# Kernel tuning notes

Measured on AMD Instinct MI355X. Metric: run time of the kernel, lower is better.

The kernel has to match this reference:

```python
import jax, jax.numpy as jnp
import numpy as np

H = 2880
E = 8
K = 2
FF = 2880
CLIP = 7.0
AUX_COEF = 0.01
INIT_STD = 0.02
B, T = 2, 1024


def setup_inputs() -> dict:
    key = jax.random.key(0)
    ks = jax.random.split(key, 4)
    x = jax.random.normal(ks[0], (B, T, H), dtype=jnp.float32)
    W_in = INIT_STD * jax.random.normal(ks[1], (E, H, 2 * FF), dtype=jnp.float32)
    b_in = jnp.zeros((E, 2 * FF), dtype=jnp.float32)
    W_out = INIT_STD * jax.random.normal(ks[2], (E, FF, H), dtype=jnp.float32)
    b_out = jnp.zeros((E, H), dtype=jnp.float32)
    router_w = INIT_STD * jax.random.normal(ks[3], (E, H), dtype=jnp.float32)
    router_b = jnp.zeros((E,), dtype=jnp.float32)
    return {"x": x, "W_in": W_in, "b_in": b_in, "W_out": W_out,
            "b_out": b_out, "router_w": router_w, "router_b": router_b}


def reference(x, W_in, b_in, W_out, b_out, router_w, router_b):
    Bx, Tx, Hx = x.shape
    x_flat = x.reshape(-1, Hx)                       # [S, H]
    logits = x_flat @ router_w.T + router_b          # [S, E]

    topk_w, topk_idx = jax.lax.top_k(logits, K)      # [S, K]
    topk_w = jax.nn.softmax(topk_w.astype(jnp.float32), axis=-1).astype(x.dtype)
    one_hot = jax.nn.one_hot(topk_idx, E, dtype=x.dtype)        # [S, K, E]
    final_w = (one_hot * topk_w[..., None]).sum(axis=1)          # [S, E]

    probs = jax.nn.softmax(logits.astype(jnp.float32), axis=-1)  # [S, E]
    importance = probs.mean(axis=0)
    load = final_w.astype(jnp.float32).mean(axis=0)
    aux_loss = AUX_COEF * E * (importance * load).sum()

    # Dense over all experts (as in the original module)
    expert_in = jnp.einsum('sh,ehd->sed', x_flat, W_in) + b_in   # [S, E, 2FF]
    up, gate = jnp.split(expert_in, 2, axis=-1)
    up = jnp.clip(up, -CLIP, CLIP)
    gate = jnp.clip(gate, -CLIP, CLIP)
    act = jax.nn.silu(gate) * up                                 # [S, E, FF]
    expert_out = jnp.einsum('sef,efh->seh', act, W_out) + b_out  # [S, E, H]
    out = jnp.einsum('seh,se->sh', expert_out, final_w).reshape(Bx, Tx, Hx)

    expert_utilization = final_w.mean(axis=0)
    router_entropy = -(probs * jnp.log(probs + 1e-10)).sum(axis=-1).mean()
    return out, aux_loss, expert_utilization, router_entropy
```

## Files before the change

kernel.cpp:

```cpp
#include <hip/hip_runtime.h>
#include <hip/hip_bf16.h>
#include <cstdint>
#include <cstddef>

#define H_ 2880
#define E_ 8
#define FF_ 2880
#define TWO_FF 5760
#define S_ 2048
#define NPAD 5120
#define CLIPV 7.0f
#define AUXC 0.01f
#define NKB 45

#define GRIDP  22112
#define GRID1C 5120
#define GRID2  640

typedef __attribute__((ext_vector_type(8))) short bf16x8;
typedef __attribute__((ext_vector_type(4))) float f32x4;

#define WS_COUNTS   0
#define WS_BASEP    64
#define WS_NS       104
#define WS_SCHED_E  128
#define WS_SCHED_C  5248
#define WS_SCHED_R  10368
#define WS_SCH2_E   15488
#define WS_SCH2_C   18048
#define WS_SCH2_R   20608
#define WS_IDX2     23168
#define WS_W2       39552
#define WS_PROBS    55936
#define WS_ENT      121472
#define WS_TOKL     129664
#define WS_ASSW     150144
#define WS_AG       262144
#define WS_TIN      29753344
#define WS_ACT      295174144
#define WS_TOUT     324665344

typedef const __attribute__((address_space(1))) void global_cvoid;
typedef __attribute__((address_space(3))) void lds_void;

__device__ __forceinline__ void gload_lds16(const void* g, void* l) {
  __builtin_amdgcn_global_load_lds((global_cvoid*)g, (lds_void*)l, 16, 0, 0);
}

__device__ __forceinline__ unsigned int pack2bf(float a, float b) {
  __hip_bfloat162 h = __float22bfloat162_rn(make_float2(a, b));
  union { __hip_bfloat162 h; unsigned int u; } c; c.h = h; return c.u;
}

__device__ __forceinline__ unsigned short f2bf1(float f) {
  __hip_bfloat16 h = __float2bfloat16(f);
  union { __hip_bfloat16 h; unsigned short u; } c; c.h = h; return c.u;
}

__device__ __forceinline__ int xcd_lid(int bid, int ns) {
  int q = ns >> 3, r = ns & 7;
  int xcd = bid & 7, i = bid >> 3;
  int cnt = q + (xcd < r ? 1 : 0);
  if (i >= cnt) return -1;
  return xcd * q + (xcd < r ? xcd : r) + i;
}

template <int LD>
__device__ __forceinline__ void convw_body(const float* __restrict__ src,
                                           unsigned short* __restrict__ dst,
                                           float (*ls)[97]) {
  int tid = threadIdx.x;
#pragma unroll
  for (int i = 0; i < 6; ++i) {
    int u = tid + 256 * i;
    int r = u / 24, c4 = u % 24;
    float4 v = *(const float4*)(src + (size_t)r * LD + c4 * 4);
    ls[r][c4 * 4 + 0] = v.x; ls[r][c4 * 4 + 1] = v.y;
    ls[r][c4 * 4 + 2] = v.z; ls[r][c4 * 4 + 3] = v.w;
  }
  __syncthreads();
#pragma unroll
  for (int i = 0; i < 3; ++i) {
    int ci = tid + 256 * i;
    int kq = ci / 96, n = ci % 96;
    float f[8];
#pragma unroll
    for (int j = 0; j < 8; ++j) f[j] = ls[kq * 8 + j][n];
    uint4 o;
    o.x = pack2bf(f[0], f[1]); o.y = pack2bf(f[2], f[3]);
    o.z = pack2bf(f[4], f[5]); o.w = pack2bf(f[6], f[7]);
    *(uint4*)(dst + ci * 8) = o;
  }
}

__global__ __launch_bounds__(256) void k_pre(
    const float* __restrict__ Win, unsigned short* __restrict__ Tin,
    const float* __restrict__ x, const float* __restrict__ rw,
    const float* __restrict__ rb, int* __restrict__ counts,
    int* __restrict__ idx2, float* __restrict__ wtop,
    float* __restrict__ probs, float* __restrict__ ent) {
  __shared__ float ls[64][97];
  int bid = blockIdx.x;
  if (bid < 21600) {
    int e = bid / 2700, r = bid % 2700, nt = r / 45, kb = r % 45;
    const float* src = Win + (size_t)e * H_ * TWO_FF + (size_t)kb * 64 * TWO_FF + nt * 96;
    unsigned short* dst = Tin + (((size_t)e * 60 + nt) * 45 + kb) * 6144;
    convw_body<TWO_FF>(src, dst, ls);
    return;
  }
  int rbid = bid - 21600;
  int wave = threadIdx.x >> 6, lane = threadIdx.x & 63;
  int s = rbid * 4 + wave;
  if (s >= S_) return;
  const float* xr = x + (size_t)s * H_;
  float acc[E_];
#pragma unroll
  for (int e = 0; e < E_; ++e) acc[e] = 0.f;
  for (int k = lane; k < H_; k += 64) {
    float xv = xr[k];
#pragma unroll
    for (int e = 0; e < E_; ++e) acc[e] = fmaf(xv, rw[e * H_ + k], acc[e]);
  }
#pragma unroll
  for (int e = 0; e < E_; ++e) {
#pragma unroll
    for (int off = 32; off > 0; off >>= 1) acc[e] += __shfl_xor(acc[e], off, 64);
    acc[e] += rb[e];
  }
  if (lane == 0) {
    int i1 = 0; float v1 = acc[0];
#pragma unroll
    for (int e = 1; e < E_; ++e) if (acc[e] > v1) { v1 = acc[e]; i1 = e; }
    int i2 = -1; float v2 = -3.4e38f;
#pragma unroll
    for (int e = 0; e < E_; ++e) if (e != i1 && acc[e] > v2) { v2 = acc[e]; i2 = e; }
    float w1 = 1.f / (1.f + expf(v2 - v1));
    float w2v = 1.f - w1;
    float m = v1;
    float se = 0.f; float p[E_];
#pragma unroll
    for (int e = 0; e < E_; ++e) { p[e] = expf(acc[e] - m); se += p[e]; }
    float inv = 1.f / se; float ents = 0.f;
#pragma unroll
    for (int e = 0; e < E_; ++e) {
      p[e] *= inv;
      ents -= p[e] * logf(p[e] + 1e-10f);
      probs[(size_t)s * E_ + e] = p[e];
    }
    ent[s] = ents;
    idx2[2 * s] = i1; idx2[2 * s + 1] = i2;
    wtop[2 * s] = w1; wtop[2 * s + 1] = w2v;
    atomicAdd(&counts[i1], 1); atomicAdd(&counts[i2], 1);
  }
}

__global__ void k_finalize(const int* __restrict__ counts, const float* __restrict__ probs,
                           const float* __restrict__ ent, const int* __restrict__ idx2,
                           const float* __restrict__ wtop, float* __restrict__ outsc,
                           int* __restrict__ basep, int* __restrict__ sched_e,
                           int* __restrict__ sched_c, int* __restrict__ sched_r,
                           int* __restrict__ s2e, int* __restrict__ s2c,
                           int* __restrict__ s2r, int* __restrict__ nsp,
                           int* __restrict__ tokl, float* __restrict__ assw) {
  __shared__ float red[256];
  __shared__ float tot[17];
  __shared__ int sh_tc[8], sh_cum[9], sh_base[9], sfill[8];
  int t = threadIdx.x;
  float imp[8], ld[8]; float es = 0.f;
#pragma unroll
  for (int e = 0; e < 8; ++e) { imp[e] = 0.f; ld[e] = 0.f; }
  for (int s = t; s < S_; s += 256) {
#pragma unroll
    for (int e = 0; e < 8; ++e) imp[e] += probs[(size_t)s * 8 + e];
    es += ent[s];
    int e0 = idx2[2 * s], e1 = idx2[2 * s + 1];
    float a = wtop[2 * s], b = wtop[2 * s + 1];
#pragma unroll
    for (int e = 0; e < 8; ++e)
      ld[e] += (e0 == e ? a : 0.f) + (e1 == e ? b : 0.f);
  }
#pragma unroll
  for (int q = 0; q < 17; ++q) {
    float v = (q < 8) ? imp[q] : ((q < 16) ? ld[q - 8] : es);
    red[t] = v; __syncthreads();
    for (int o = 128; o > 0; o >>= 1) { if (t < o) red[t] += red[t + o]; __syncthreads(); }
    if (t == 0) tot[q] = red[0];
    __syncthreads();
  }
  if (t == 0) {
    float aux = 0.f;
#pragma unroll
    for (int e = 0; e < 8; ++e) aux += (tot[e] / (float)S_) * (tot[8 + e] / (float)S_);
    aux *= AUXC * (float)E_;
    outsc[0] = aux;
#pragma unroll
    for (int e = 0; e < 8; ++e) outsc[1 + e] = tot[8 + e] / (float)S_;
    outsc[9] = tot[16] / (float)S_;
    int bp = 0, cum = 0;
    for (int e = 0; e < 8; ++e) {
      int tc = (counts[e] + 127) >> 7;
      sh_tc[e] = tc; sh_cum[e] = cum; sh_base[e] = bp;
      basep[e] = bp;
      cum += tc; bp += tc << 7;
    }
    sh_cum[8] = cum; sh_base[8] = bp; basep[8] = bp;
    nsp[0] = cum * 30; nsp[1] = cum * 15;
  }
  if (t < 8) sfill[t] = 0;
  __syncthreads();
  int ntile = sh_cum[8];
  int ns1 = ntile * 30;
  for (int sidx = t; sidx < ns1; sidx += 256) {
    int e = 0;
    while (e < 7 && sidx >= sh_cum[e + 1] * 30) ++e;
    int tc = sh_tc[e];
    int rem = sidx - sh_cum[e] * 30;
    int col = rem / tc, tt = rem - col * tc;
    sched_e[sidx] = e; sched_c[sidx] = col; sched_r[sidx] = tt * 128;
  }
  int ns2 = ntile * 15;
  for (int sidx = t; sidx < ns2; sidx += 256) {
    int e = 0;
    while (e < 7 && sidx >= sh_cum[e + 1] * 15) ++e;
    int tc = sh_tc[e];
    int rem = sidx - sh_cum[e] * 15;
    int col = rem / tc, tt = rem - col * tc;
    s2e[sidx] = e; s2c[sidx] = col; s2r[sidx] = tt * 128;
  }
  for (int s = t; s < S_; s += 256) {
#pragma unroll
    for (int k = 0; k < 2; ++k) {
      int e = idx2[2 * s + k];
      int p = sh_base[e] + atomicAdd(&sfill[e], 1);
      tokl[p] = s;
      assw[p] = wtop[2 * s + k];
    }
  }
}

__global__ void k_gather(const float* __restrict__ x, const int* __restrict__ tokl,
                         unsigned short* __restrict__ Ag) {
  int g = blockIdx.x;
  int tok = tokl[g];
  int tm = g >> 7, r = g & 127;
  unsigned short* dst = Ag + (size_t)tm * 45 * 8192;
  const float* src = x + (size_t)tok * H_;
  for (int c = threadIdx.x; c < 360; c += 256) {
    float4 v0 = *(const float4*)(src + c * 8);
    float4 v1 = *(const float4*)(src + c * 8 + 4);
    uint4 o;
    o.x = pack2bf(v0.x, v0.y); o.y = pack2bf(v0.z, v0.w);
    o.z = pack2bf(v1.x, v1.y); o.w = pack2bf(v1.z, v1.w);
    *(uint4*)(dst + (size_t)(c >> 3) * 8192 + (c & 7) * 1024 + r * 8) = o;
  }
}

__global__ __launch_bounds__(256, 2) void k_gemm1c(
    const unsigned short* __restrict__ Ag, const unsigned short* __restrict__ Tin,
    const float* __restrict__ bin, const int* __restrict__ sched_e,
    const int* __restrict__ sched_c, const int* __restrict__ sched_r,
    const int* __restrict__ basep, const int* __restrict__ counts,
    const int* __restrict__ nsp, unsigned short* __restrict__ act,
    const float* __restrict__ Wout, unsigned short* __restrict__ Tout) {
  __shared__ __align__(16) char lds[81920];
  int bid = blockIdx.x;
  int g = bid >> 5, p = bid & 31, phase = g & 3;
  if ((p & 3) != phase) {
    int nless = (p >> 2) + (((p & 3) > phase) ? 1 : 0);
    int cid = g * 24 + (p - nless);
    float (*ls)[97] = (float(*)[97])lds;
    for (int tile = cid; tile < 10800; tile += 3840) {
      int e = tile / 1350, r2 = tile % 1350, nt = r2 / 45, kb = r2 % 45;
      const float* src = Wout + (size_t)e * FF_ * H_ + (size_t)kb * 64 * H_ + nt * 96;
      unsigned short* dst = Tout + (((size_t)e * 30 + nt) * 45 + kb) * 6144;
      convw_body<H_>(src, dst, ls);
      __syncthreads();
    }
    return;
  }
  int lid = g * 8 + (p >> 2);
  if (lid >= nsp[0]) return;
  int e = sched_e[lid], col = sched_c[lid], row0 = sched_r[lid];
  int n_e = counts[e], rbase = basep[e];
  int n0 = col * 96;
  int tid = threadIdx.x, lane = tid & 63, wv = tid >> 6;
  int wm = wv >> 1, wn = wv & 1;
  int tile_m = (rbase + row0) >> 7;

  const char* abase  = (const char*)Ag  + (size_t)tile_m * 45 * 16384;
  const char* bubase = (const char*)Tin + (((size_t)e * 60 + col) * 45) * 12288;
  const char* bgbase = (const char*)Tin + (((size_t)e * 60 + col + 30) * 45) * 12288;

#define ST1(BUF, KT) do {                                                        \
  const char* at_ = abase + (size_t)(KT) * 16384;                                \
  const char* bu_ = bubase + (size_t)(KT) * 12288;                               \
  const char* bg_ = bgbase + (size_t)(KT) * 12288;                               \
  _Pragma("unroll") for (int i_ = 0; i_ < 4; ++i_)                               \
    gload_lds16(at_ + (wv * 4 + i_) * 1024 + lane * 16,                          \
                lds + (BUF) * 16384 + (wv * 4 + i_) * 1024);                     \
  _Pragma("unroll") for (int i_ = 0; i_ < 3; ++i_) {                             \
    gload_lds16(bu_ + (wv * 3 + i_) * 1024 + lane * 16,                          \
                lds + 32768 + (BUF) * 12288 + (wv * 3 + i_) * 1024);             \
    gload_lds16(bg_ + (wv * 3 + i_) * 1024 + lane * 16,                          \
                lds + 57344 + (BUF) * 12288 + (wv * 3 + i_) * 1024); }           \
} while (0)

  f32x4 aU[4][3], aG[4][3];
#pragma unroll
  for (int m = 0; m < 4; ++m)
#pragma unroll
    for (int n = 0; n < 3; ++n) { aU[m][n] = (f32x4)0.f; aG[m][n] = (f32x4)0.f; }

  ST1(0, 0);
  int cur = 0;
  for (int kt = 0; kt < NKB; ++kt) {
    asm volatile("s_barrier" ::: "memory");
    if (kt + 1 < NKB) {
      ST1(cur ^ 1, kt + 1);
      asm volatile("s_waitcnt vmcnt(10)" ::: "memory");
    } else {
      asm volatile("s_waitcnt vmcnt(0)" ::: "memory");
    }
    asm volatile("s_barrier" ::: "memory");
    const char* Ab  = lds + cur * 16384 + (lane >> 4) * 2048 + (wm * 64 + (lane & 15)) * 16;
    const char* Bub = lds + 32768 + cur * 12288 + (lane >> 4) * 1536 + (wn * 48 + (lane & 15)) * 16;
    const char* Bgb = Bub + 24576;
#pragma unroll
    for (int s = 0; s < 2; ++s) {
      bf16x8 af[4], bu[3], bg[3];
#pragma unroll
      for (int m = 0; m < 4; ++m) af[m] = *(const bf16x8*)(Ab + s * 8192 + m * 256);
#pragma unroll
      for (int n = 0; n < 3; ++n) {
        bu[n] = *(const bf16x8*)(Bub + s * 6144 + n * 256);
        bg[n] = *(const bf16x8*)(Bgb + s * 6144 + n * 256);
      }
#pragma unroll
      for (int n = 0; n < 3; ++n)
#pragma unroll
        for (int m = 0; m < 4; ++m) {
          aU[m][n] = __builtin_amdgcn_mfma_f32_16x16x32_bf16(af[m], bu[n], aU[m][n], 0, 0, 0);
          aG[m][n] = __builtin_amdgcn_mfma_f32_16x16x32_bf16(af[m], bg[n], aG[m][n], 0, 0, 0);
        }
    }
    cur ^= 1;
  }
#undef ST1

  float bias_u[3], bias_g[3];
#pragma unroll
  for (int n = 0; n < 3; ++n) {
    int cidx = n0 + wn * 48 + n * 16 + (lane & 15);
    bias_u[n] = bin[(size_t)e * TWO_FF + cidx];
    bias_g[n] = bin[(size_t)e * TWO_FF + FF_ + cidx];
  }
  unsigned short* atile = act + (size_t)tile_m * 45 * 8192;
#pragma unroll
  for (int m = 0; m < 4; ++m) {
#pragma unroll
    for (int q = 0; q < 4; ++q) {
      int r = wm * 64 + m * 16 + (lane >> 4) * 4 + q;
      if (row0 + r < n_e) {
#pragma unroll
        for (int n = 0; n < 3; ++n) {
          int cidx = n0 + wn * 48 + n * 16 + (lane & 15);
          float u = aU[m][n][q] + bias_u[n];
          float gg = aG[m][n][q] + bias_g[n];
          u = fminf(fmaxf(u, -CLIPV), CLIPV);
          gg = fminf(fmaxf(gg, -CLIPV), CLIPV);
          float sig = 1.f / (1.f + expf(-gg));
          atile[(size_t)(cidx >> 6) * 8192 + ((cidx >> 3) & 7) * 1024 + r * 8 + (cidx & 7)]
              = f2bf1(gg * sig * u);
        }
      }
    }
  }
}

__global__ __launch_bounds__(256, 2) void k_gemm2(
    const unsigned short* __restrict__ act, const unsigned short* __restrict__ Tout,
    const float* __restrict__ bout, const int* __restrict__ s2e,
    const int* __restrict__ s2c, const int* __restrict__ s2r,
    const int* __restrict__ basep, const int* __restrict__ counts,
    const int* __restrict__ nsp, const int* __restrict__ tokl,
    const float* __restrict__ assw, float* __restrict__ out) {
  __shared__ __align__(16) char lds[81920];
  int lid = xcd_lid(blockIdx.x, nsp[1]);
  if (lid < 0) return;
  int e = s2e[lid], col = s2c[lid], row0 = s2r[lid];
  int n_e = counts[e], rbase = basep[e];
  int n0 = col * 192;
  int tid = threadIdx.x, lane = tid & 63, wv = tid >> 6;
  int wm = wv >> 1, wn = wv & 1;
  int tile_m = (rbase + row0) >> 7;

  const char* abase = (const char*)act + (size_t)tile_m * 45 * 16384;
  const char* bbase = (const char*)Tout + (((size_t)e * 30 + col * 2) * 45) * 12288;

#define ST2(BUF, KT) do {                                                        \
  const char* at_ = abase + (size_t)(KT) * 16384;                                \
  _Pragma("unroll") for (int i_ = 0; i_ < 4; ++i_)                               \
    gload_lds16(at_ + (wv * 4 + i_) * 1024 + lane * 16,                          \
                lds + (BUF) * 16384 + (wv * 4 + i_) * 1024);                     \
  _Pragma("unroll") for (int i_ = 0; i_ < 6; ++i_) {                             \
    int ch_ = wv * 6 + i_;                                                       \
    const char* bt_ = bbase + (size_t)(ch_ / 12) * 45 * 12288                    \
                      + (size_t)(KT) * 12288 + (ch_ % 12) * 1024;                \
    gload_lds16(bt_ + lane * 16, lds + 32768 + (BUF) * 24576 + ch_ * 1024); }    \
} while (0)

  f32x4 acc[4][6];
#pragma unroll
  for (int m = 0; m < 4; ++m)
#pragma unroll
    for (int n = 0; n < 6; ++n) acc[m][n] = (f32x4)0.f;

  ST2(0, 0);
  int cur = 0;
  for (int kt = 0; kt < NKB; ++kt) {
    asm volatile("s_barrier" ::: "memory");
    if (kt + 1 < NKB) {
      ST2(cur ^ 1, kt + 1);
      asm volatile("s_waitcnt vmcnt(10)" ::: "memory");
    } else {
      asm volatile("s_waitcnt vmcnt(0)" ::: "memory");
    }
    asm volatile("s_barrier" ::: "memory");
    const char* Ab = lds + cur * 16384 + (lane >> 4) * 2048 + (wm * 64 + (lane & 15)) * 16;
    const char* Bb = lds + 32768 + cur * 24576 + wn * 12288 + (lane >> 4) * 1536 + (lane & 15) * 16;
#pragma unroll
    for (int s = 0; s < 2; ++s) {
      bf16x8 af[4], bf[6];
#pragma unroll
      for (int m = 0; m < 4; ++m) af[m] = *(const bf16x8*)(Ab + s * 8192 + m * 256);
#pragma unroll
      for (int n = 0; n < 6; ++n) bf[n] = *(const bf16x8*)(Bb + s * 6144 + n * 256);
#pragma unroll
      for (int n = 0; n < 6; ++n)
#pragma unroll
        for (int m = 0; m < 4; ++m)
          acc[m][n] = __builtin_amdgcn_mfma_f32_16x16x32_bf16(af[m], bf[n], acc[m][n], 0, 0, 0);
    }
    cur ^= 1;
  }
#undef ST2

  float bb[6];
#pragma unroll
  for (int n = 0; n < 6; ++n)
    bb[n] = bout[(size_t)e * H_ + n0 + wn * 96 + n * 16 + (lane & 15)];
#pragma unroll
  for (int m = 0; m < 4; ++m) {
#pragma unroll
    for (int q = 0; q < 4; ++q) {
      int r = wm * 64 + m * 16 + (lane >> 4) * 4 + q;
      if (row0 + r < n_e) {
        int g = rbase + row0 + r;
        int tok = tokl[g];
        float w = assw[g];
        float* orow = out + (size_t)tok * H_;
#pragma unroll
        for (int n = 0; n < 6; ++n) {
          int cidx = n0 + wn * 96 + n * 16 + (lane & 15);
          atomicAdd(&orow[cidx], w * (acc[m][n][q] + bb[n]));
        }
      }
    }
  }
}

extern "C" void kernel_launch(void* const* d_in, const int* in_sizes, int n_in,
                              void* d_out, int out_size, void* d_ws, size_t ws_size,
                              hipStream_t stream) {
  (void)in_sizes; (void)n_in; (void)ws_size;
  const float* x        = (const float*)d_in[0];
  const float* W_in     = (const float*)d_in[1];
  const float* b_in     = (const float*)d_in[2];
  const float* W_out    = (const float*)d_in[3];
  const float* b_out    = (const float*)d_in[4];
  const float* router_w = (const float*)d_in[5];
  const float* router_b = (const float*)d_in[6];
  float* out = (float*)d_out;
  char* ws = (char*)d_ws;

  int*   counts  = (int*)(ws + WS_COUNTS);
  int*   basep   = (int*)(ws + WS_BASEP);
  int*   nsp     = (int*)(ws + WS_NS);
  int*   sched_e = (int*)(ws + WS_SCHED_E);
  int*   sched_c = (int*)(ws + WS_SCHED_C);
  int*   sched_r = (int*)(ws + WS_SCHED_R);
  int*   s2e     = (int*)(ws + WS_SCH2_E);
  int*   s2c     = (int*)(ws + WS_SCH2_C);
  int*   s2r     = (int*)(ws + WS_SCH2_R);
  int*   idx2    = (int*)(ws + WS_IDX2);
  float* wtop    = (float*)(ws + WS_W2);
  float* probs   = (float*)(ws + WS_PROBS);
  float* ent     = (float*)(ws + WS_ENT);
  int*   tokl    = (int*)(ws + WS_TOKL);
  float* assw    = (float*)(ws + WS_ASSW);
  unsigned short* Ag   = (unsigned short*)(ws + WS_AG);
  unsigned short* Tin  = (unsigned short*)(ws + WS_TIN);
  unsigned short* actp = (unsigned short*)(ws + WS_ACT);
  unsigned short* Tout = (unsigned short*)(ws + WS_TOUT);

  hipMemsetAsync(ws + WS_COUNTS, 0, 128, stream);
  hipMemsetAsync(ws + WS_TOKL, 0, NPAD * 4, stream);
  hipMemsetAsync(d_out, 0, (size_t)out_size * sizeof(float), stream);

  k_pre<<<GRIDP, 256, 0, stream>>>(W_in, Tin, x, router_w, router_b,
                                   counts, idx2, wtop, probs, ent);
  k_finalize<<<1, 256, 0, stream>>>(counts, probs, ent, idx2, wtop,
                                    out + (size_t)S_ * H_, basep,
                                    sched_e, sched_c, sched_r,
                                    s2e, s2c, s2r, nsp, tokl, assw);
  k_gather<<<NPAD, 256, 0, stream>>>(x, tokl, Ag);
  k_gemm1c<<<GRID1C, 256, 0, stream>>>(Ag, Tin, b_in, sched_e, sched_c, sched_r,
                                       basep, counts, nsp, actp, W_out, Tout);
  k_gemm2<<<GRID2, 256, 0, stream>>>(actp, Tout, b_out, s2e, s2c, s2r,
                                     basep, counts, nsp, tokl, assw, out);
}
```

Baseline: 647.9 us.

## Fuse token gather into GEMM1 loads and drop separate gather kernel

Converts all tokens of x to a bf16 tiled layout inside the pre-kernel, then has GEMM1 gather rows by token index directly during its global-to-LDS loads, which removes the separate gather kernel launch. The W_out conversion blocks become one tile per block, with the GEMM1 grid enlarged to hold them, instead of a strided loop. It also raises wave priority around the MFMA loops in both GEMMs and merges the workspace memsets. Risks are scattered per-row A loads that coalesce less well, and padded rows that read token 0 through the zeroed token list.

New measurement: 708.0 us. 9.3% more time.

```diff
diff --git a/kernel.cpp b/kernel.cpp
--- a/kernel.cpp
+++ b/kernel.cpp
@@ -13,8 +13,8 @@
 #define AUXC 0.01f
 #define NKB 45
 
-#define GRIDP  22112
-#define GRID1C 5120
+#define GRIDP  24160
+#define GRID1C 14400
 #define GRID2  640
 
 typedef __attribute__((ext_vector_type(8))) short bf16x8;
@@ -98,19 +98,35 @@
     const float* __restrict__ x, const float* __restrict__ rw,
     const float* __restrict__ rb, int* __restrict__ counts,
     int* __restrict__ idx2, float* __restrict__ wtop,
-    float* __restrict__ probs, float* __restrict__ ent) {
+    float* __restrict__ probs, float* __restrict__ ent,
+    unsigned short* __restrict__ AgT) {
   __shared__ float ls[64][97];
   int bid = blockIdx.x;
-  if (bid < 21600) {
-    int e = bid / 2700, r = bid % 2700, nt = r / 45, kb = r % 45;
+  if (bid >= 2560) {
+    int cid = bid - 2560;
+    int e = cid / 2700, r = cid % 2700, nt = r / 45, kb = r % 45;
     const float* src = Win + (size_t)e * H_ * TWO_FF + (size_t)kb * 64 * TWO_FF + nt * 96;
     unsigned short* dst = Tin + (((size_t)e * 60 + nt) * 45 + kb) * 6144;
     convw_body<TWO_FF>(src, dst, ls);
     return;
   }
-  int rbid = bid - 21600;
+  if (bid >= 512) {
+    int t = bid - 512;
+    int tm = t >> 7, r = t & 127;
+    unsigned short* dst = AgT + (size_t)tm * 45 * 8192;
+    const float* src = x + (size_t)t * H_;
+    for (int c = threadIdx.x; c < 360; c += 256) {
+      float4 v0 = *(const float4*)(src + c * 8);
+      float4 v1 = *(const float4*)(src + c * 8 + 4);
+      uint4 o;
+      o.x = pack2bf(v0.x, v0.y); o.y = pack2bf(v0.z, v0.w);
+      o.z = pack2bf(v1.x, v1.y); o.w = pack2bf(v1.z, v1.w);
+      *(uint4*)(dst + (size_t)(c >> 3) * 8192 + (c & 7) * 1024 + r * 8) = o;
+    }
+    return;
+  }
   int wave = threadIdx.x >> 6, lane = threadIdx.x & 63;
-  int s = rbid * 4 + wave;
+  int s = bid * 4 + wave;
   if (s >= S_) return;
   const float* xr = x + (size_t)s * H_;
   float acc[E_];
@@ -238,29 +254,13 @@
   }
 }
 
-__global__ void k_gather(const float* __restrict__ x, const int* __restrict__ tokl,
-                         unsigned short* __restrict__ Ag) {
-  int g = blockIdx.x;
-  int tok = tokl[g];
-  int tm = g >> 7, r = g & 127;
-  unsigned short* dst = Ag + (size_t)tm * 45 * 8192;
-  const float* src = x + (size_t)tok * H_;
-  for (int c = threadIdx.x; c < 360; c += 256) {
-    float4 v0 = *(const float4*)(src + c * 8);
-    float4 v1 = *(const float4*)(src + c * 8 + 4);
-    uint4 o;
-    o.x = pack2bf(v0.x, v0.y); o.y = pack2bf(v0.z, v0.w);
-    o.z = pack2bf(v1.x, v1.y); o.w = pack2bf(v1.z, v1.w);
-    *(uint4*)(dst + (size_t)(c >> 3) * 8192 + (c & 7) * 1024 + r * 8) = o;
-  }
-}
-
 __global__ __launch_bounds__(256, 2) void k_gemm1c(
-    const unsigned short* __restrict__ Ag, const unsigned short* __restrict__ Tin,
+    const unsigned short* __restrict__ AgT, const unsigned short* __restrict__ Tin,
     const float* __restrict__ bin, const int* __restrict__ sched_e,
     const int* __restrict__ sched_c, const int* __restrict__ sched_r,
     const int* __restrict__ basep, const int* __restrict__ counts,
-    const int* __restrict__ nsp, unsigned short* __restrict__ act,
+    const int* __restrict__ nsp, const int* __restrict__ tokl,
+    unsigned short* __restrict__ act,
     const float* __restrict__ Wout, unsigned short* __restrict__ Tout) {
   __shared__ __align__(16) char lds[81920];
   int bid = blockIdx.x;
@@ -268,14 +268,12 @@
   if ((p & 3) != phase) {
     int nless = (p >> 2) + (((p & 3) > phase) ? 1 : 0);
     int cid = g * 24 + (p - nless);
+    if (cid >= 10800) return;
     float (*ls)[97] = (float(*)[97])lds;
-    for (int tile = cid; tile < 10800; tile += 3840) {
-      int e = tile / 1350, r2 = tile % 1350, nt = r2 / 45, kb = r2 % 45;
-      const float* src = Wout + (size_t)e * FF_ * H_ + (size_t)kb * 64 * H_ + nt * 96;
-      unsigned short* dst = Tout + (((size_t)e * 30 + nt) * 45 + kb) * 6144;
-      convw_body<H_>(src, dst, ls);
-      __syncthreads();
-    }
+    int e = cid / 1350, r2 = cid % 1350, nt = r2 / 45, kb = r2 % 45;
+    const float* src = Wout + (size_t)e * FF_ * H_ + (size_t)kb * 64 * H_ + nt * 96;
+    unsigned short* dst = Tout + (((size_t)e * 30 + nt) * 45 + kb) * 6144;
+    convw_body<H_>(src, dst, ls);
     return;
   }
   int lid = g * 8 + (p >> 2);
@@ -287,16 +285,24 @@
   int wm = wv >> 1, wn = wv & 1;
   int tile_m = (rbase + row0) >> 7;
 
-  const char* abase  = (const char*)Ag  + (size_t)tile_m * 45 * 16384;
+  int tok0 = tokl[rbase + row0 + lane];
+  int tok1 = tokl[rbase + row0 + 64 + lane];
+  const char* AgB = (const char*)AgT;
+  const char* asrc[4];
+#pragma unroll
+  for (int i = 0; i < 4; ++i) {
+    int u = wv * 4 + i, kq = u >> 1, rh = u & 1;
+    int tk = rh ? tok1 : tok0;
+    asrc[i] = AgB + (size_t)(tk >> 7) * 737280 + (size_t)(tk & 127) * 16 + kq * 2048;
+  }
   const char* bubase = (const char*)Tin + (((size_t)e * 60 + col) * 45) * 12288;
   const char* bgbase = (const char*)Tin + (((size_t)e * 60 + col + 30) * 45) * 12288;
 
 #define ST1(BUF, KT) do {                                                        \
-  const char* at_ = abase + (size_t)(KT) * 16384;                                \
   const char* bu_ = bubase + (size_t)(KT) * 12288;                               \
   const char* bg_ = bgbase + (size_t)(KT) * 12288;                               \
   _Pragma("unroll") for (int i_ = 0; i_ < 4; ++i_)                               \
-    gload_lds16(at_ + (wv * 4 + i_) * 1024 + lane * 16,                          \
+    gload_lds16(asrc[i_] + (size_t)(KT) * 16384,                                 \
                 lds + (BUF) * 16384 + (wv * 4 + i_) * 1024);                     \
   _Pragma("unroll") for (int i_ = 0; i_ < 3; ++i_) {                             \
     gload_lds16(bu_ + (wv * 3 + i_) * 1024 + lane * 16,                          \
@@ -325,6 +331,7 @@
     const char* Ab  = lds + cur * 16384 + (lane >> 4) * 2048 + (wm * 64 + (lane & 15)) * 16;
     const char* Bub = lds + 32768 + cur * 12288 + (lane >> 4) * 1536 + (wn * 48 + (lane & 15)) * 16;
     const char* Bgb = Bub + 24576;
+    __builtin_amdgcn_s_setprio(1);
 #pragma unroll
     for (int s = 0; s < 2; ++s) {
       bf16x8 af[4], bu[3], bg[3];
@@ -343,6 +350,7 @@
           aG[m][n] = __builtin_amdgcn_mfma_f32_16x16x32_bf16(af[m], bg[n], aG[m][n], 0, 0, 0);
         }
     }
+    __builtin_amdgcn_s_setprio(0);
     cur ^= 1;
   }
 #undef ST1
@@ -428,6 +436,7 @@
     asm volatile("s_barrier" ::: "memory");
     const char* Ab = lds + cur * 16384 + (lane >> 4) * 2048 + (wm * 64 + (lane & 15)) * 16;
     const char* Bb = lds + 32768 + cur * 24576 + wn * 12288 + (lane >> 4) * 1536 + (lane & 15) * 16;
+    __builtin_amdgcn_s_setprio(1);
 #pragma unroll
     for (int s = 0; s < 2; ++s) {
       bf16x8 af[4], bf[6];
@@ -441,6 +450,7 @@
         for (int m = 0; m < 4; ++m)
           acc[m][n] = __builtin_amdgcn_mfma_f32_16x16x32_bf16(af[m], bf[n], acc[m][n], 0, 0, 0);
     }
+    __builtin_amdgcn_s_setprio(0);
     cur ^= 1;
   }
 #undef ST2
@@ -498,24 +508,22 @@
   float* ent     = (float*)(ws + WS_ENT);
   int*   tokl    = (int*)(ws + WS_TOKL);
   float* assw    = (float*)(ws + WS_ASSW);
-  unsigned short* Ag   = (unsigned short*)(ws + WS_AG);
+  unsigned short* AgT  = (unsigned short*)(ws + WS_AG);
   unsigned short* Tin  = (unsigned short*)(ws + WS_TIN);
   unsigned short* actp = (unsigned short*)(ws + WS_ACT);
   unsigned short* Tout = (unsigned short*)(ws + WS_TOUT);
 
-  hipMemsetAsync(ws + WS_COUNTS, 0, 128, stream);
-  hipMemsetAsync(ws + WS_TOKL, 0, NPAD * 4, stream);
+  hipMemsetAsync(ws, 0, WS_ASSW, stream);
   hipMemsetAsync(d_out, 0, (size_t)out_size * sizeof(float), stream);
 
   k_pre<<<GRIDP, 256, 0, stream>>>(W_in, Tin, x, router_w, router_b,
-                                   counts, idx2, wtop, probs, ent);
+                                   counts, idx2, wtop, probs, ent, AgT);
   k_finalize<<<1, 256, 0, stream>>>(counts, probs, ent, idx2, wtop,
                                     out + (size_t)S_ * H_, basep,
                                     sched_e, sched_c, sched_r,
                                     s2e, s2c, s2r, nsp, tokl, assw);
-  k_gather<<<NPAD, 256, 0, stream>>>(x, tokl, Ag);
-  k_gemm1c<<<GRID1C, 256, 0, stream>>>(Ag, Tin, b_in, sched_e, sched_c, sched_r,
-                                       basep, counts, nsp, actp, W_out, Tout);
+  k_gemm1c<<<GRID1C, 256, 0, stream>>>(AgT, Tin, b_in, sched_e, sched_c, sched_r,
+                                       basep, counts, nsp, tokl, actp, W_out, Tout);
   k_gemm2<<<GRID2, 256, 0, stream>>>(actp, Tout, b_out, s2e, s2c, s2r,
                                      basep, counts, nsp, tokl, assw, out);
 }
```
